# Optimization experiments

Hardware: AMD Instinct MI355X
Metric: run time of the kernel (lower is better)

## Reference

```python
import jax, jax.numpy as jnp
import numpy as np

# Config (matches init_kwargs defaults): V=25 joints, C=16 -> D=400, heads=2,
# ffn=64*25=1600, window L=9, stride=1, postnorm, gelu, dropout ignored (eval).
N, C, T, V = 16, 16, 300, 25
D = C * V          # 400
H = 2              # nhead
FF = 64 * V        # 1600
L = 9              # trans_length
MAX_LEN = 301


def _layernorm(x, g, b, eps=1e-5):
    mu = jnp.mean(x, axis=-1, keepdims=True)
    var = jnp.mean(jnp.square(x - mu), axis=-1, keepdims=True)
    return (x - mu) * jax.lax.rsqrt(var + eps) * g + b


def setup_inputs() -> dict:
    key = jax.random.key(0)
    ks = jax.random.split(key, 12)
    s = 0.02
    return {
        "x": jax.random.normal(ks[0], (N, C, T, V), jnp.float32),
        "pe": jax.random.normal(ks[1], (1, MAX_LEN, D), jnp.float32) * s,
        "w_in": jax.random.normal(ks[2], (3 * D, D), jnp.float32) * s,
        "b_in": jnp.zeros((3 * D,), jnp.float32),
        "w_out": jax.random.normal(ks[3], (D, D), jnp.float32) * s,
        "b_out": jnp.zeros((D,), jnp.float32),
        "w1": jax.random.normal(ks[4], (FF, D), jnp.float32) * s,
        "b1": jnp.zeros((FF,), jnp.float32),
        "w2": jax.random.normal(ks[5], (D, FF), jnp.float32) * s,
        "b2": jnp.zeros((D,), jnp.float32),
        "ln1_g": jnp.ones((D,), jnp.float32),
        "ln1_b": jnp.zeros((D,), jnp.float32),
        "ln2_g": jnp.ones((D,), jnp.float32),
        "ln2_b": jnp.zeros((D,), jnp.float32),
    }


def _encoder_layer(h, w_in, b_in, w_out, b_out, w1, b1, w2, b2,
                   ln1_g, ln1_b, ln2_g, ln2_b):
    # h: [B, L, D]; post-norm TransformerEncoderLayer (torch default)
    B, Lw, Dm = h.shape
    dh = Dm // H
    qkv = h @ w_in.T + b_in                             # [B,L,3D]
    q, k, v = jnp.split(qkv, 3, axis=-1)
    def heads(t):
        return t.reshape(B, Lw, H, dh).transpose(0, 2, 1, 3)  # [B,H,L,dh]
    q, k, v = heads(q), heads(k), heads(v)
    scores = jnp.einsum('bhqd,bhkd->bhqk', q, k) / np.float32(np.sqrt(dh))
    att = jax.nn.softmax(scores, axis=-1)
    o = jnp.einsum('bhqk,bhkd->bhqd', att, v)
    o = o.transpose(0, 2, 1, 3).reshape(B, Lw, Dm) @ w_out.T + b_out
    h = _layernorm(h + o, ln1_g, ln1_b)
    ff = jax.nn.gelu(h @ w1.T + b1, approximate=False) @ w2.T + b2
    return _layernorm(h + ff, ln2_g, ln2_b)


def reference(x, pe, w_in, b_in, w_out, b_out, w1, b1, w2, b2,
              ln1_g, ln1_b, ln2_g, ln2_b):
    n, c, t, v = x.shape
    d = c * v
    # [N,C,T,V] -> [N,T,V,C] -> [N,T,D]  (flatten order is (V,C), as in torch view)
    xs = x.transpose(0, 2, 3, 1).reshape(n, t, d)
    xs = xs + pe[:, :t, :]
    W = t - L                                            # number of windows (stride=1)
    win = jnp.arange(W)
    idx = win[:, None] + jnp.arange(L)[None, :]          # [W,L] gather indices
    xw = xs[:, idx, :].reshape(n * W, L, d)              # batched windows
    out = _encoder_layer(xw, w_in, b_in, w_out, b_out, w1, b1, w2, b2,
                         ln1_g, ln1_b, ln2_g, ln2_b)
    out = out.reshape(n, W * L, d)
    # window i writes into rows i//2 : i//2 + L and results are summed
    pos = ((win // 2)[:, None] + jnp.arange(L)[None, :]).reshape(-1)  # [W*L]
    xt = jnp.zeros((n, t, d), xs.dtype).at[:, pos, :].add(out)
    # [N,T,D] -> [N,T,V,C] -> [N,C,T,V]
    return xt.reshape(n, t, v, c).transpose(0, 3, 1, 2)
```

## Files before the change

kernel.cpp:

```cpp
#include <hip/hip_runtime.h>
#include <cstdint>
#include <cstddef>

#define N_    16
#define C_    16
#define T_    300
#define V_    25
#define D_    400
#define H_    2
#define DH_   200
#define FF_   1600
#define L_    9
#define W_    291
#define NW_   (N_*W_)
#define NT_   (N_*T_)

#define KP_   416
#define SD_   400
#define SQKV_ 1200
#define SFF_  1600

#define WIN_OFF   0u
#define WOUT_OFF  1064960u
#define W1_OFF    1490944u
#define W2_OFF    2981888u
#define XS_OFF    4620288u
#define QKV_OFF   8511488u
#define Z_OFF     20185088u
#define HEAD_END  53708288u

#define WAIT_VM3   0xF73
#define WAIT_VM0   0xF70

using u16 = unsigned short;
using u32 = unsigned int;
using frag  = __attribute__((ext_vector_type(8))) short;
using f32x4 = __attribute__((ext_vector_type(4))) float;

__device__ __forceinline__ float bf2f(u16 u){
  return __uint_as_float(((u32)u) << 16);
}
__device__ __forceinline__ u16 f2bf(float f){
  return (u16)((__float_as_uint(f) + 0x8000u) >> 16);
}
__device__ __forceinline__ u16 f2h(float f){
  _Float16 h = (_Float16)f;
  return *(u16*)&h;
}
__device__ __forceinline__ float h2f(u16 u){
  _Float16 h = *(_Float16*)&u;
  return (float)h;
}
__device__ __forceinline__ float gelu_f(float v){
  float s = __expf(-1.702f * v);
  return v * __builtin_amdgcn_rcpf(1.f + s);
}
__device__ __forceinline__ void unpack8(uint4 v, float* o){
  o[0] = bf2f((u16)(v.x & 0xffffu)); o[1] = bf2f((u16)(v.x >> 16));
  o[2] = bf2f((u16)(v.y & 0xffffu)); o[3] = bf2f((u16)(v.y >> 16));
  o[4] = bf2f((u16)(v.z & 0xffffu)); o[5] = bf2f((u16)(v.z >> 16));
  o[6] = bf2f((u16)(v.w & 0xffffu)); o[7] = bf2f((u16)(v.w >> 16));
}

__device__ __forceinline__ void convw_body(const float* src, u16* dst,
                                           int dN, int dK, int sN, int sK, int idx){
  if (idx >= dN * dK) return;
  int n = idx / dK, k = idx % dK;
  dst[idx] = (n < sN && k < sK) ? f2bf(src[(size_t)n * sK + k]) : (u16)0;
}

#define PREP_GRID 13824
__global__ __launch_bounds__(256) void prep_kernel(const float* __restrict__ x,
                                                   const float* __restrict__ pe,
                                                   const float* __restrict__ w_in,
                                                   const float* __restrict__ w_out,
                                                   const float* __restrict__ w1,
                                                   const float* __restrict__ w2,
                                                   u16* __restrict__ xs,
                                                   u16* __restrict__ w_in_b,
                                                   u16* __restrict__ w_out_b,
                                                   u16* __restrict__ w1_b,
                                                   u16* __restrict__ w2_b){
  __shared__ float xv[400];
  int b = blockIdx.x;
  int tid = threadIdx.x;
  if (b < 4800){
    int t = b % T_, n = b / T_;
    for (int i = tid; i < 400; i += 256){
      int c = i / 25, v = i - c*25;
      xv[i] = x[(((size_t)(n*C_ + c))*T_ + t)*V_ + v];
    }
    __syncthreads();
    for (int d = tid; d < 400; d += 256){
      float val = xv[(d & 15)*25 + (d >> 4)] + pe[t*D_ + d];
      xs[(size_t)b * D_ + d] = f2bf(val);
    }
  } else if (b < 6880){
    convw_body(w_in,  w_in_b,  1280, KP_, 1200, D_,  (b - 4800) * 256 + tid);
  } else if (b < 7712){
    convw_body(w_out, w_out_b,  512, KP_,  400, D_,  (b - 6880) * 256 + tid);
  } else if (b < 10624){
    convw_body(w1,    w1_b,   1792, KP_, 1600, D_,  (b - 7712) * 256 + tid);
  } else {
    convw_body(w2,    w2_b,    512, SFF_, 400, FF_, (b - 10624) * 256 + tid);
  }
}

template<int ACT>
__global__ __launch_bounds__(512) void gemm_mfma(const u16* __restrict__ A, int lda,
                                                 const u16* __restrict__ B, int ldb,
                                                 const float* __restrict__ bias,
                                                 u16* __restrict__ C, int ldc,
                                                 int Nn, int KPd,
                                                 int gx, int gy){
  __shared__ u16 smem[36864];
  int id = blockIdx.x;
  int c  = id & 7, t = id >> 3;
  int bx = t % gx;
  int by = (t / gx) * 8 + c;
  if (by >= gy) return;
  const int m0 = by * 128, n0 = bx * 256;

  const int tid  = threadIdx.x;
  const int lane = tid & 63;
  const int wv   = tid >> 6;
  const int quad = lane >> 4, l16 = lane & 15;
  const int wm   = wv & 1,   wn  = wv >> 1;

  const int srow = tid >> 2;
  const int sseg = (tid & 3) ^ ((tid >> 3) & 3);
  const u16* Ag = A + (size_t)(m0 + srow) * lda + sseg*8;
  const u16* Bg = B + (size_t)(n0 + srow) * ldb + sseg*8;

  f32x4 acc[4][4] = {};
  const int sa = quad ^ ((l16 >> 1) & 3);

  auto stage = [&](int buf, int kt){
    __builtin_amdgcn_global_load_lds(
        (const __attribute__((address_space(1))) void*)(Ag + kt),
        (__attribute__((address_space(3))) void*)(&smem[buf*4096 + wv*512]), 16, 0, 0);
    __builtin_amdgcn_global_load_lds(
        (const __attribute__((address_space(1))) void*)(Bg + kt),
        (__attribute__((address_space(3))) void*)(&smem[12288 + buf*8192 + wv*512]), 16, 0, 0);
    __builtin_amdgcn_global_load_lds(
        (const __attribute__((address_space(1))) void*)(Bg + kt + (size_t)128*ldb),
        (__attribute__((address_space(3))) void*)(&smem[12288 + buf*8192 + 4096 + wv*512]), 16, 0, 0);
  };

  const int nit = KPd >> 5;
  stage(0, 0);
  stage(1, 32);
  int nb = 2;
  for (int it = 0; it < nit; ++it){
    if (it < nit - 1) __builtin_amdgcn_s_waitcnt(WAIT_VM3);
    else              __builtin_amdgcn_s_waitcnt(WAIT_VM0);
    __builtin_amdgcn_s_barrier();
    if (it + 2 < nit){
      stage(nb, (it + 2) << 5);
      nb = (nb == 2) ? 0 : nb + 1;
    }
    const int buf = it % 3;
    const u16* Ar = &smem[buf*4096];
    const u16* Br = &smem[12288 + buf*8192];
    frag af[4], bfr[4];
    #pragma unroll
    for (int i = 0; i < 4; ++i)
      af[i]  = *(const frag*)(&Ar[(wm*64 + i*16 + l16)*32 + sa*8]);
    #pragma unroll
    for (int j = 0; j < 4; ++j)
      bfr[j] = *(const frag*)(&Br[(wn*64 + j*16 + l16)*32 + sa*8]);
    #pragma unroll
    for (int i = 0; i < 4; ++i)
      #pragma unroll
      for (int j = 0; j < 4; ++j)
        acc[i][j] = __builtin_amdgcn_mfma_f32_16x16x32_bf16(af[i], bfr[j], acc[i][j], 0, 0, 0);
  }

  __builtin_amdgcn_s_barrier();

  u16* ep = &smem[wv * 4608];
  #pragma unroll
  for (int j = 0; j < 4; ++j){
    int n = n0 + wn*64 + j*16 + l16;
    float bj = (n < Nn) ? bias[n] : 0.f;
    #pragma unroll
    for (int i = 0; i < 4; ++i){
      #pragma unroll
      for (int r = 0; r < 4; ++r){
        float v = acc[i][j][r] + bj;
        if (ACT) v = gelu_f(v);
        ep[(i*16 + quad*4 + r)*72 + j*16 + l16] = f2bf(v);
      }
    }
  }
  #pragma unroll
  for (int p = 0; p < 8; ++p){
    int row = p*8 + (lane >> 3);
    int seg = lane & 7;
    int nc  = n0 + wn*64 + seg*8;
    if (nc < Nn){
      uint4 v = *(const uint4*)(&ep[row*72 + seg*8]);
      *(uint4*)(C + (size_t)(m0 + wm*64 + row)*ldc + nc) = v;
    }
  }
}

__global__ __launch_bounds__(512) void gemm_ff2(const u16* __restrict__ A, int lda,
                                                const u16* __restrict__ B, int ldb,
                                                const float* __restrict__ bias,
                                                u16* __restrict__ C0, u16* __restrict__ C1,
                                                int ldc, int Nn, int KH,
                                                int gx, int gy, int Mr){
  __shared__ u16 smem[36864];
  int id = blockIdx.x;
  int c  = id & 7, t = id >> 3;
  int bxp = t % (2*gx);
  int by  = (t / (2*gx)) * 8 + c;
  if (by >= gy) return;
  const int half = (bxp >= gx) ? 1 : 0;
  const int bx   = bxp - half*gx;
  const int m0 = by * 128, n0 = bx * 256;
  const int koff = half * KH;
  u16* C = half ? C1 : C0;

  const int tid  = threadIdx.x;
  const int lane = tid & 63;
  const int wv   = tid >> 6;
  const int quad = lane >> 4, l16 = lane & 15;
  const int wm   = wv & 1,   wn  = wv >> 1;

  const int srow = tid >> 2;
  const int sseg = (tid & 3) ^ ((tid >> 3) & 3);
  const u16* Ag = A + (size_t)(m0 + srow) * lda + koff + sseg*8;
  const u16* Bg = B + (size_t)(n0 + srow) * ldb + koff + sseg*8;

  f32x4 acc[4][4] = {};
  const int sa = quad ^ ((l16 >> 1) & 3);

  auto stage = [&](int buf, int kt){
    __builtin_amdgcn_global_load_lds(
        (const __attribute__((address_space(1))) void*)(Ag + kt),
        (__attribute__((address_space(3))) void*)(&smem[buf*4096 + wv*512]), 16, 0, 0);
    __builtin_amdgcn_global_load_lds(
        (const __attribute__((address_space(1))) void*)(Bg + kt),
        (__attribute__((address_space(3))) void*)(&smem[12288 + buf*8192 + wv*512]), 16, 0, 0);
    __builtin_amdgcn_global_load_lds(
        (const __attribute__((address_space(1))) void*)(Bg + kt + (size_t)128*ldb),
        (__attribute__((address_space(3))) void*)(&smem[12288 + buf*8192 + 4096 + wv*512]), 16, 0, 0);
  };

  const int nit = KH >> 5;
  stage(0, 0);
  stage(1, 32);
  int nb = 2;
  for (int it = 0; it < nit; ++it){
    if (it < nit - 1) __builtin_amdgcn_s_waitcnt(WAIT_VM3);
    else              __builtin_amdgcn_s_waitcnt(WAIT_VM0);
    __builtin_amdgcn_s_barrier();
    if (it + 2 < nit){
      stage(nb, (it + 2) << 5);
      nb = (nb == 2) ? 0 : nb + 1;
    }
    const int buf = it % 3;
    const u16* Ar = &smem[buf*4096];
    const u16* Br = &smem[12288 + buf*8192];
    frag af[4], bfr[4];
    #pragma unroll
    for (int i = 0; i < 4; ++i)
      af[i]  = *(const frag*)(&Ar[(wm*64 + i*16 + l16)*32 + sa*8]);
    #pragma unroll
    for (int j = 0; j < 4; ++j)
      bfr[j] = *(const frag*)(&Br[(wn*64 + j*16 + l16)*32 + sa*8]);
    #pragma unroll
    for (int i = 0; i < 4; ++i)
      #pragma unroll
      for (int j = 0; j < 4; ++j)
        acc[i][j] = __builtin_amdgcn_mfma_f32_16x16x32_bf16(af[i], bfr[j], acc[i][j], 0, 0, 0);
  }

  __builtin_amdgcn_s_barrier();

  u16* ep = &smem[wv * 4608];
  #pragma unroll
  for (int j = 0; j < 4; ++j){
    int n = n0 + wn*64 + j*16 + l16;
    float bj = (!half && n < Nn) ? bias[n] : 0.f;
    #pragma unroll
    for (int i = 0; i < 4; ++i){
      #pragma unroll
      for (int r = 0; r < 4; ++r){
        float v = acc[i][j][r] + bj;
        ep[(i*16 + quad*4 + r)*72 + j*16 + l16] = f2bf(v);
      }
    }
  }
  #pragma unroll
  for (int p = 0; p < 8; ++p){
    int row = p*8 + (lane >> 3);
    int seg = lane & 7;
    int nc  = n0 + wn*64 + seg*8;
    int mr  = m0 + wm*64 + row;
    if (nc < Nn && mr < Mr){
      uint4 v = *(const uint4*)(&ep[row*72 + seg*8]);
      *(uint4*)(C + (size_t)mr*ldc + nc) = v;
    }
  }
}

#define WB_     8
#define ATT_NB  37
#define ATT_GRID (N_ * ATT_NB)
__global__ __launch_bounds__(256) void attn_kernel(const u16* __restrict__ qkv,
                                                   u16* __restrict__ o,
                                                   int g0, int gend){
  __shared__ u16 kv[20480];
  __shared__ float att[WB_ * 2 * 81];
  const int b  = blockIdx.x;
  const int n  = b / ATT_NB;
  const int w0 = (b - n * ATT_NB) * WB_;
  const int gbase = n * W_ + w0;
  if (gbase >= gend || gbase + WB_ <= g0) return;

  const int tid  = threadIdx.x;
  const int lane = tid & 63;
  const int wv   = tid >> 6;

  const char* gsrc = (const char*)(qkv + (size_t)(n * T_ + w0) * SQKV_);
  #pragma unroll
  for (int j = 0; j < 10; ++j){
    __builtin_amdgcn_global_load_lds(
        (const __attribute__((address_space(1))) void*)(gsrc + j*4096 + wv*1024 + lane*16),
        (__attribute__((address_space(3))) void*)((char*)kv + j*4096 + wv*1024),
        16, 0, 0);
  }
  __builtin_amdgcn_s_waitcnt(WAIT_VM0);
  __syncthreads();

  for (int i = tid; i < WB_ * 162; i += 256){
    int w  = i / 162;
    int r  = i - w * 162;
    int h  = r / 81;
    int p  = r - h * 81;
    int qi = p / 9, ki = p - qi * 9;
    const u16* qp = kv + (w + qi) * 1200 + h * DH_;
    const u16* kp = kv + (w + ki) * 1200 + D_ + h * DH_;
    float s = 0.f;
    #pragma unroll 5
    for (int cch = 0; cch < 25; ++cch){
      float qa[8], kb[8];
      unpack8(*(const uint4*)(qp + cch*8), qa);
      unpack8(*(const uint4*)(kp + cch*8), kb);
      #pragma unroll
      for (int e = 0; e < 8; ++e) s += qa[e] * kb[e];
    }
    att[i] = s * 0.07071067811865475f;
  }
  __syncthreads();

  if (tid < WB_ * 18){
    float* row = att + tid * 9;
    float mx = row[0];
    #pragma unroll
    for (int j = 1; j < 9; ++j) mx = fmaxf(mx, row[j]);
    float e[9]; float sum = 0.f;
    #pragma unroll
    for (int j = 0; j < 9; ++j){ e[j] = __expf(row[j] - mx); sum += e[j]; }
    float inv = 1.f / sum;
    #pragma unroll
    for (int j = 0; j < 9; ++j) row[j] = e[j] * inv;
  }
  __syncthreads();

  for (int i = tid; i < WB_ * 900; i += 256){
    int w  = i / 900;
    int r  = i - w * 900;
    int l  = r / 100;
    int c4 = r - l * 100;
    int h  = (c4 >= 50) ? 1 : 0;
    const float* ap = att + (w*2 + h)*81 + l*9;
    float o4[4] = {0.f, 0.f, 0.f, 0.f};
    #pragma unroll
    for (int ki = 0; ki < 9; ++ki){
      float a = ap[ki];
      uint2 vv = *(const uint2*)(kv + (w + ki)*1200 + 2*D_ + c4*4);
      o4[0] += a * bf2f((u16)(vv.x & 0xffffu));
      o4[1] += a * bf2f((u16)(vv.x >> 16));
      o4[2] += a * bf2f((u16)(vv.y & 0xffffu));
      o4[3] += a * bf2f((u16)(vv.y >> 16));
    }
    int g = gbase + w;
    if (w0 + w < W_ && g >= g0 && g < gend){
      u32 lo = (u32)f2bf(o4[0]) | ((u32)f2bf(o4[1]) << 16);
      u32 hi = (u32)f2bf(o4[2]) | ((u32)f2bf(o4[3]) << 16);
      *(uint2*)(o + ((size_t)(g - g0) * L_ + l) * SD_ + c4*4) = make_uint2(lo, hi);
    }
  }
}

__global__ __launch_bounds__(256) void ln1_kernel(const u16* __restrict__ y,
                                                  const float* __restrict__ gam,
                                                  const float* __restrict__ bet,
                                                  u16* __restrict__ out,
                                                  const u16* __restrict__ xs,
                                                  int g0){
  const int wv = threadIdx.x >> 6, lane = threadIdx.x & 63;
  const int r = blockIdx.x * 4 + wv;
  const int g = g0 + r / L_, l = r % L_;
  const int n = g / W_, w = g % W_;
  const u16* arow = xs + ((size_t)(n*T_ + w + l)) * SD_;
  const u16* brow = y + (size_t)r * SD_;

  const bool act = lane < 50;
  float v[8];
  float s = 0.f, s2 = 0.f;
  if (act){
    float a8[8], b8[8];
    unpack8(*(const uint4*)(arow + lane*8), a8);
    unpack8(*(const uint4*)(brow + lane*8), b8);
    #pragma unroll
    for (int i = 0; i < 8; ++i){ v[i] = a8[i] + b8[i]; s += v[i]; s2 += v[i]*v[i]; }
  } else {
    #pragma unroll
    for (int i = 0; i < 8; ++i) v[i] = 0.f;
  }
  #pragma unroll
  for (int off = 32; off; off >>= 1){
    s  += __shfl_xor(s,  off);
    s2 += __shfl_xor(s2, off);
  }
  float mean = s * (1.f / D_);
  float rstd = rsqrtf(s2 * (1.f / D_) - mean*mean + 1e-5f);
  if (act){
    float4 ga = *(const float4*)(gam + lane*8);
    float4 gb = *(const float4*)(gam + lane*8 + 4);
    float4 ba = *(const float4*)(bet + lane*8);
    float4 bb = *(const float4*)(bet + lane*8 + 4);
    float gg[8] = {ga.x,ga.y,ga.z,ga.w, gb.x,gb.y,gb.z,gb.w};
    float bb8[8]= {ba.x,ba.y,ba.z,ba.w, bb.x,bb.y,bb.z,bb.w};
    u32 o4[4];
    #pragma unroll
    for (int i = 0; i < 4; ++i){
      u16 lo = f2bf((v[2*i]   - mean) * rstd * gg[2*i]   + bb8[2*i]);
      u16 hi = f2bf((v[2*i+1] - mean) * rstd * gg[2*i+1] + bb8[2*i+1]);
      o4[i] = (u32)lo | ((u32)hi << 16);
    }
    *(uint4*)(out + (size_t)r * SD_ + lane*8) = make_uint4(o4[0],o4[1],o4[2],o4[3]);
  }
}

__global__ __launch_bounds__(256) void ln2_gather(const u16* __restrict__ h,
                                                  const u16* __restrict__ y,
                                                  const u16* __restrict__ y2,
                                                  const float* __restrict__ gam,
                                                  const float* __restrict__ bet,
                                                  float* __restrict__ dout){
  __shared__ float buf[4][400];
  const int b = blockIdx.x;
  const int t = b % T_;
  const int n = b / T_;
  const int wv = threadIdx.x >> 6, lane = threadIdx.x & 63;
  const bool act = lane < 50;

  float gg[8], bb8[8];
  if (act){
    float4 ga = *(const float4*)(gam + lane*8);
    float4 gb = *(const float4*)(gam + lane*8 + 4);
    float4 ba = *(const float4*)(bet + lane*8);
    float4 bb = *(const float4*)(bet + lane*8 + 4);
    gg[0]=ga.x; gg[1]=ga.y; gg[2]=ga.z; gg[3]=ga.w;
    gg[4]=gb.x; gg[5]=gb.y; gg[6]=gb.z; gg[7]=gb.w;
    bb8[0]=ba.x; bb8[1]=ba.y; bb8[2]=ba.z; bb8[3]=ba.w;
    bb8[4]=bb.x; bb8[5]=bb.y; bb8[6]=bb.z; bb8[7]=bb.w;
  }
  float racc[8] = {0.f,0.f,0.f,0.f,0.f,0.f,0.f,0.f};

  for (int idx = wv; idx < 18; idx += 4){
    int l  = idx >> 1;
    int dt = t - l;
    if (dt < 0 || dt > 145) continue;
    int w = dt * 2 + (idx & 1);
    if (w >= W_) continue;
    size_t r = ((size_t)(n * W_ + w)) * L_ + l;
    const u16* arow = h + r * SD_;
    const u16* brow = y + r * SD_;
    const u16* crow = y2 + r * SD_;
    float v[8];
    float s = 0.f, s2 = 0.f;
    if (act){
      float a8[8], b8[8], c8[8];
      unpack8(*(const uint4*)(arow + lane*8), a8);
      unpack8(*(const uint4*)(brow + lane*8), b8);
      unpack8(*(const uint4*)(crow + lane*8), c8);
      #pragma unroll
      for (int i = 0; i < 8; ++i){ v[i] = a8[i] + b8[i] + c8[i]; s += v[i]; s2 += v[i]*v[i]; }
    } else {
      #pragma unroll
      for (int i = 0; i < 8; ++i) v[i] = 0.f;
    }
    #pragma unroll
    for (int off = 32; off; off >>= 1){
      s  += __shfl_xor(s,  off);
      s2 += __shfl_xor(s2, off);
    }
    float mean = s * (1.f / D_);
    float rstd = rsqrtf(s2 * (1.f / D_) - mean*mean + 1e-5f);
    if (act){
      #pragma unroll
      for (int i = 0; i < 8; ++i)
        racc[i] += (v[i] - mean) * rstd * gg[i] + bb8[i];
    }
  }
  if (act){
    #pragma unroll
    for (int i = 0; i < 8; ++i) buf[wv][lane*8 + i] = racc[i];
  }
  __syncthreads();
  for (int d = threadIdx.x; d < D_; d += 256){
    float s = buf[0][d] + buf[1][d] + buf[2][d] + buf[3][d];
    dout[(((size_t)(n*C_ + (d & 15)))*T_ + t)*V_ + (d >> 4)] = s;
  }
}

__global__ __launch_bounds__(256) void ln2z_kernel(const u16* __restrict__ h,
                                                   const u16* __restrict__ y,
                                                   const float* __restrict__ gam,
                                                   const float* __restrict__ bet,
                                                   u16* __restrict__ z,
                                                   int g0){
  const int wv = threadIdx.x >> 6, lane = threadIdx.x & 63;
  const int r = blockIdx.x * 4 + wv;
  const u16* arow = h + (size_t)r * SD_;
  const u16* brow = y + (size_t)r * SD_;

  const bool act = lane < 50;
  float v[8];
  float s = 0.f, s2 = 0.f;
  if (act){
    float a8[8], b8[8];
    unpack8(*(const uint4*)(arow + lane*8), a8);
    unpack8(*(const uint4*)(brow + lane*8), b8);
    #pragma unroll
    for (int i = 0; i < 8; ++i){ v[i] = a8[i] + b8[i]; s += v[i]; s2 += v[i]*v[i]; }
  } else {
    #pragma unroll
    for (int i = 0; i < 8; ++i) v[i] = 0.f;
  }
  #pragma unroll
  for (int off = 32; off; off >>= 1){
    s  += __shfl_xor(s,  off);
    s2 += __shfl_xor(s2, off);
  }
  float mean = s * (1.f / D_);
  float rstd = rsqrtf(s2 * (1.f / D_) - mean*mean + 1e-5f);
  if (act){
    float4 ga = *(const float4*)(gam + lane*8);
    float4 gb = *(const float4*)(gam + lane*8 + 4);
    float4 ba = *(const float4*)(bet + lane*8);
    float4 bb = *(const float4*)(bet + lane*8 + 4);
    float gg[8] = {ga.x,ga.y,ga.z,ga.w, gb.x,gb.y,gb.z,gb.w};
    float bb8[8]= {ba.x,ba.y,ba.z,ba.w, bb.x,bb.y,bb.z,bb.w};
    u32 o4[4];
    #pragma unroll
    for (int i = 0; i < 4; ++i){
      u16 lo = f2h((v[2*i]   - mean) * rstd * gg[2*i]   + bb8[2*i]);
      u16 hi = f2h((v[2*i+1] - mean) * rstd * gg[2*i+1] + bb8[2*i+1]);
      o4[i] = (u32)lo | ((u32)hi << 16);
    }
    *(uint4*)(z + ((size_t)(g0 * L_) + r) * SD_ + lane*8) = make_uint4(o4[0],o4[1],o4[2],o4[3]);
  }
}

__global__ __launch_bounds__(256) void gather_final(const u16* __restrict__ z,
                                                    float* __restrict__ dout){
  int idx = blockIdx.x * 256 + threadIdx.x;
  if (idx >= NT_ * D_) return;
  int d  = idx % D_;
  int nt = idx / D_;
  int t  = nt % T_;
  int n  = nt / T_;
  float s = 0.f;
  #pragma unroll
  for (int l = 0; l < L_; ++l){
    int dt = t - l;
    if (dt >= 0 && dt <= 145){
      int w = dt * 2;
      const u16* zp = z + ((size_t)((n*W_ + w)*L_ + l)) * SD_ + d;
      s += h2f(zp[0]);
      if (w + 1 < W_) s += h2f(zp[(size_t)L_ * SD_]);
    }
  }
  dout[(((size_t)(n*C_ + (d & 15)))*T_ + t)*V_ + (d >> 4)] = s;
}

extern "C" void kernel_launch(void* const* d_in, const int* in_sizes, int n_in,
                              void* d_out, int out_size, void* d_ws, size_t ws_size,
                              hipStream_t stream){
  (void)in_sizes; (void)n_in; (void)out_size;
  const float* x     = (const float*)d_in[0];
  const float* pe    = (const float*)d_in[1];
  const float* w_in  = (const float*)d_in[2];
  const float* b_in  = (const float*)d_in[3];
  const float* w_out = (const float*)d_in[4];
  const float* b_out = (const float*)d_in[5];
  const float* w1    = (const float*)d_in[6];
  const float* b1    = (const float*)d_in[7];
  const float* w2    = (const float*)d_in[8];
  const float* b2    = (const float*)d_in[9];
  const float* ln1g  = (const float*)d_in[10];
  const float* ln1b  = (const float*)d_in[11];
  const float* ln2g  = (const float*)d_in[12];
  const float* ln2b  = (const float*)d_in[13];

  int nch = 3;
  {
    size_t need1 = (size_t)HEAD_END + (size_t)41984 * 4800;
    size_t need2 = (size_t)HEAD_END + (size_t)20992 * 4800;
    if (ws_size >= need1 + (1u<<20)) nch = 1;
    else if (ws_size >= need2 + (1u<<20)) nch = 2;
  }
  const int CW  = NW_ / nch;
  const int RC  = CW * L_;
  const int RCP = ((RC + 127) / 128) * 128;

  char* ws = (char*)d_ws;
  u16*   w_in_b  = (u16*)(ws + WIN_OFF);
  u16*   w_out_b = (u16*)(ws + WOUT_OFF);
  u16*   w1_b    = (u16*)(ws + W1_OFF);
  u16*   w2_b    = (u16*)(ws + W2_OFF);
  u16*   xs      = (u16*)(ws + XS_OFF);
  u16*   qkv     = (u16*)(ws + QKV_OFF);
  u16*   z       = (u16*)(ws + Z_OFF);
  u16*   y2      = (u16*)(ws + Z_OFF);
  u16*   y_c     = (u16*)(ws + HEAD_END);
  u16*   h_c     = y_c + (size_t)RCP * SD_;
  u16*   ffc     = h_c + (size_t)RCP * SD_;
  u16*   o_c     = ffc;

  prep_kernel<<<PREP_GRID, 256, 0, stream>>>(x, pe, w_in, w_out, w1, w2,
                                             xs, w_in_b, w_out_b, w1_b, w2_b);

  {
    int gx = 5, gy = (NT_ + 127)/128, gy8 = (gy + 7) & ~7;
    gemm_mfma<0><<<gx*gy8, 512, 0, stream>>>(
        xs, SD_, w_in_b, KP_, b_in, qkv, SQKV_, 1200, KP_, gx, gy);
  }

  const int gyc = RCP/128, gyc8 = (gyc + 7) & ~7;

  for (int g0 = 0; g0 < NW_; g0 += CW){
    attn_kernel<<<ATT_GRID, 256, 0, stream>>>(qkv, o_c, g0, g0 + CW);

    gemm_mfma<0><<<2*gyc8, 512, 0, stream>>>(
        o_c, SD_, w_out_b, KP_, b_out, y_c, SD_, D_, KP_, 2, gyc);

    ln1_kernel<<<RC/4, 256, 0, stream>>>(y_c, ln1g, ln1b, h_c, xs, g0);

    gemm_mfma<1><<<7*gyc8, 512, 0, stream>>>(
        h_c, SD_, w1_b, KP_, b1, ffc, SFF_, FF_, KP_, 7, gyc);

    if (nch == 1){
      gemm_ff2<<<4*gyc8, 512, 0, stream>>>(
          ffc, SFF_, w2_b, SFF_, b2, y_c, y2, SD_, D_, 800, 2, gyc, RC);
    } else {
      gemm_mfma<0><<<2*gyc8, 512, 0, stream>>>(
          ffc, SFF_, w2_b, SFF_, b2, y_c, SD_, D_, SFF_, 2, gyc);
      ln2z_kernel<<<RC/4, 256, 0, stream>>>(h_c, y_c, ln2g, ln2b, z, g0);
    }
  }

  if (nch == 1)
    ln2_gather<<<NT_, 256, 0, stream>>>(h_c, y_c, y2, ln2g, ln2b, (float*)d_out);
  else
    gather_final<<<(NT_*D_ + 255)/256, 256, 0, stream>>>(z, (float*)d_out);
}
```

Measured before the change: 364.5 us.

## Fuse out-projection GEMM with residual LayerNorm; drop split-K FF2 path

Replaces the split-K FF2 kernel with a new kernel that computes the attention output projection over full 128x512 tiles (all 400 columns per block), stages the result in LDS and applies residual add with xs plus LayerNorm1 in the epilogue. This removes the y_c round trip and the separate ln1 launch. The FF2 GEMM reverts to the plain non-split kernel, so ln2_gather now reads two inputs instead of three. The fused kernel uses more LDS and fewer, larger blocks, which lowers occupancy, and dropping split-K may cost FF2 parallelism.

```diff
diff --git a/kernel.cpp b/kernel.cpp
--- a/kernel.cpp
+++ b/kernel.cpp
@@ -29,6 +29,7 @@
 #define Z_OFF     20185088u
 #define HEAD_END  53708288u
 
+#define WAIT_VM10  0xF7A
 #define WAIT_VM3   0xF73
 #define WAIT_VM0   0xF70
 
@@ -205,23 +206,20 @@
   }
 }
 
-__global__ __launch_bounds__(512) void gemm_ff2(const u16* __restrict__ A, int lda,
-                                                const u16* __restrict__ B, int ldb,
-                                                const float* __restrict__ bias,
-                                                u16* __restrict__ C0, u16* __restrict__ C1,
-                                                int ldc, int Nn, int KH,
-                                                int gx, int gy, int Mr){
-  __shared__ u16 smem[36864];
+__global__ __launch_bounds__(512) void gemm_wout_ln1(const u16* __restrict__ A, int lda,
+                                                     const u16* __restrict__ B, int ldb,
+                                                     const float* __restrict__ bias,
+                                                     const u16* __restrict__ xs,
+                                                     const float* __restrict__ gam,
+                                                     const float* __restrict__ bet,
+                                                     u16* __restrict__ hout,
+                                                     int Mr, int KPd, int gy){
+  __shared__ u16 smem[61440];
   int id = blockIdx.x;
   int c  = id & 7, t = id >> 3;
-  int bxp = t % (2*gx);
-  int by  = (t / (2*gx)) * 8 + c;
+  int by = t * 8 + c;
   if (by >= gy) return;
-  const int half = (bxp >= gx) ? 1 : 0;
-  const int bx   = bxp - half*gx;
-  const int m0 = by * 128, n0 = bx * 256;
-  const int koff = half * KH;
-  u16* C = half ? C1 : C0;
+  const int m0 = by * 128;
 
   const int tid  = threadIdx.x;
   const int lane = tid & 63;
@@ -231,30 +229,30 @@
 
   const int srow = tid >> 2;
   const int sseg = (tid & 3) ^ ((tid >> 3) & 3);
-  const u16* Ag = A + (size_t)(m0 + srow) * lda + koff + sseg*8;
-  const u16* Bg = B + (size_t)(n0 + srow) * ldb + koff + sseg*8;
-
-  f32x4 acc[4][4] = {};
+  const u16* Ag = A + (size_t)(m0 + srow) * lda + sseg*8;
+  const u16* Bg = B + (size_t)srow * ldb + sseg*8;
+
+  f32x4 acc[4][8] = {};
   const int sa = quad ^ ((l16 >> 1) & 3);
 
   auto stage = [&](int buf, int kt){
     __builtin_amdgcn_global_load_lds(
         (const __attribute__((address_space(1))) void*)(Ag + kt),
         (__attribute__((address_space(3))) void*)(&smem[buf*4096 + wv*512]), 16, 0, 0);
-    __builtin_amdgcn_global_load_lds(
-        (const __attribute__((address_space(1))) void*)(Bg + kt),
-        (__attribute__((address_space(3))) void*)(&smem[12288 + buf*8192 + wv*512]), 16, 0, 0);
-    __builtin_amdgcn_global_load_lds(
-        (const __attribute__((address_space(1))) void*)(Bg + kt + (size_t)128*ldb),
-        (__attribute__((address_space(3))) void*)(&smem[12288 + buf*8192 + 4096 + wv*512]), 16, 0, 0);
+    #pragma unroll
+    for (int ch = 0; ch < 4; ++ch){
+      __builtin_amdgcn_global_load_lds(
+          (const __attribute__((address_space(1))) void*)(Bg + kt + (size_t)(128*ch)*ldb),
+          (__attribute__((address_space(3))) void*)(&smem[12288 + buf*16384 + ch*4096 + wv*512]), 16, 0, 0);
+    }
   };
 
-  const int nit = KH >> 5;
+  const int nit = KPd >> 5;
   stage(0, 0);
   stage(1, 32);
   int nb = 2;
   for (int it = 0; it < nit; ++it){
-    if (it < nit - 1) __builtin_amdgcn_s_waitcnt(WAIT_VM3);
+    if (it < nit - 1) __builtin_amdgcn_s_waitcnt(WAIT_VM10);
     else              __builtin_amdgcn_s_waitcnt(WAIT_VM0);
     __builtin_amdgcn_s_barrier();
     if (it + 2 < nit){
@@ -263,46 +261,91 @@
     }
     const int buf = it % 3;
     const u16* Ar = &smem[buf*4096];
-    const u16* Br = &smem[12288 + buf*8192];
-    frag af[4], bfr[4];
+    const u16* Br = &smem[12288 + buf*16384];
+    frag af[4];
     #pragma unroll
     for (int i = 0; i < 4; ++i)
-      af[i]  = *(const frag*)(&Ar[(wm*64 + i*16 + l16)*32 + sa*8]);
-    #pragma unroll
-    for (int j = 0; j < 4; ++j)
-      bfr[j] = *(const frag*)(&Br[(wn*64 + j*16 + l16)*32 + sa*8]);
-    #pragma unroll
-    for (int i = 0; i < 4; ++i)
+      af[i] = *(const frag*)(&Ar[(wm*64 + i*16 + l16)*32 + sa*8]);
+    #pragma unroll
+    for (int jh = 0; jh < 2; ++jh){
+      frag bfr[4];
       #pragma unroll
       for (int j = 0; j < 4; ++j)
-        acc[i][j] = __builtin_amdgcn_mfma_f32_16x16x32_bf16(af[i], bfr[j], acc[i][j], 0, 0, 0);
+        bfr[j] = *(const frag*)(&Br[(wn*128 + (jh*4+j)*16 + l16)*32 + sa*8]);
+      #pragma unroll
+      for (int i = 0; i < 4; ++i)
+        #pragma unroll
+        for (int j = 0; j < 4; ++j)
+          acc[i][jh*4+j] = __builtin_amdgcn_mfma_f32_16x16x32_bf16(af[i], bfr[j], acc[i][jh*4+j], 0, 0, 0);
+    }
   }
 
   __builtin_amdgcn_s_barrier();
 
-  u16* ep = &smem[wv * 4608];
+  u16* ep = smem;
   #pragma unroll
-  for (int j = 0; j < 4; ++j){
-    int n = n0 + wn*64 + j*16 + l16;
-    float bj = (!half && n < Nn) ? bias[n] : 0.f;
-    #pragma unroll
-    for (int i = 0; i < 4; ++i){
-      #pragma unroll
-      for (int r = 0; r < 4; ++r){
-        float v = acc[i][j][r] + bj;
-        ep[(i*16 + quad*4 + r)*72 + j*16 + l16] = f2bf(v);
+  for (int j = 0; j < 8; ++j){
+    int nc = wn*128 + j*16 + l16;
+    if (nc < 400){
+      float bj = bias[nc];
+      #pragma unroll
+      for (int i = 0; i < 4; ++i){
+        #pragma unroll
+        for (int r = 0; r < 4; ++r){
+          ep[(wm*64 + i*16 + quad*4 + r)*408 + nc] = f2bf(acc[i][j][r] + bj);
+        }
       }
     }
   }
-  #pragma unroll
-  for (int p = 0; p < 8; ++p){
-    int row = p*8 + (lane >> 3);
-    int seg = lane & 7;
-    int nc  = n0 + wn*64 + seg*8;
-    int mr  = m0 + wm*64 + row;
-    if (nc < Nn && mr < Mr){
-      uint4 v = *(const uint4*)(&ep[row*72 + seg*8]);
-      *(uint4*)(C + (size_t)mr*ldc + nc) = v;
+  __syncthreads();
+
+  const bool act = lane < 50;
+  float gg[8], bb8[8];
+  if (act){
+    float4 ga = *(const float4*)(gam + lane*8);
+    float4 gb = *(const float4*)(gam + lane*8 + 4);
+    float4 ba = *(const float4*)(bet + lane*8);
+    float4 bb = *(const float4*)(bet + lane*8 + 4);
+    gg[0]=ga.x; gg[1]=ga.y; gg[2]=ga.z; gg[3]=ga.w;
+    gg[4]=gb.x; gg[5]=gb.y; gg[6]=gb.z; gg[7]=gb.w;
+    bb8[0]=ba.x; bb8[1]=ba.y; bb8[2]=ba.z; bb8[3]=ba.w;
+    bb8[4]=bb.x; bb8[5]=bb.y; bb8[6]=bb.z; bb8[7]=bb.w;
+  }
+  for (int rr = 0; rr < 16; ++rr){
+    int row = wv*16 + rr;
+    int rg  = m0 + row;
+    if (rg >= Mr) break;
+    int g = rg / L_, l = rg - g*L_;
+    int n = g / W_, w = g - n*W_;
+    const u16* arow = xs + ((size_t)(n*T_ + w + l)) * SD_;
+    float v[8];
+    float s = 0.f, s2 = 0.f;
+    if (act){
+      float a8[8], b8[8];
+      unpack8(*(const uint4*)(arow + lane*8), a8);
+      unpack8(*(const uint4*)(&ep[row*408 + lane*8]), b8);
+      #pragma unroll
+      for (int i = 0; i < 8; ++i){ v[i] = a8[i] + b8[i]; s += v[i]; s2 += v[i]*v[i]; }
+    } else {
+      #pragma unroll
+      for (int i = 0; i < 8; ++i) v[i] = 0.f;
+    }
+    #pragma unroll
+    for (int off = 32; off; off >>= 1){
+      s  += __shfl_xor(s,  off);
+      s2 += __shfl_xor(s2, off);
+    }
+    float mean = s * (1.f / D_);
+    float rstd = rsqrtf(s2 * (1.f / D_) - mean*mean + 1e-5f);
+    if (act){
+      u32 o4[4];
+      #pragma unroll
+      for (int i = 0; i < 4; ++i){
+        u16 lo = f2bf((v[2*i]   - mean) * rstd * gg[2*i]   + bb8[2*i]);
+        u16 hi = f2bf((v[2*i+1] - mean) * rstd * gg[2*i+1] + bb8[2*i+1]);
+        o4[i] = (u32)lo | ((u32)hi << 16);
+      }
+      *(uint4*)(hout + (size_t)rg * SD_ + lane*8) = make_uint4(o4[0],o4[1],o4[2],o4[3]);
     }
   }
 }
@@ -450,7 +493,6 @@
 
 __global__ __launch_bounds__(256) void ln2_gather(const u16* __restrict__ h,
                                                   const u16* __restrict__ y,
-                                                  const u16* __restrict__ y2,
                                                   const float* __restrict__ gam,
                                                   const float* __restrict__ bet,
                                                   float* __restrict__ dout){
@@ -483,16 +525,14 @@
     size_t r = ((size_t)(n * W_ + w)) * L_ + l;
     const u16* arow = h + r * SD_;
     const u16* brow = y + r * SD_;
-    const u16* crow = y2 + r * SD_;
     float v[8];
     float s = 0.f, s2 = 0.f;
     if (act){
-      float a8[8], b8[8], c8[8];
+      float a8[8], b8[8];
       unpack8(*(const uint4*)(arow + lane*8), a8);
       unpack8(*(const uint4*)(brow + lane*8), b8);
-      unpack8(*(const uint4*)(crow + lane*8), c8);
-      #pragma unroll
-      for (int i = 0; i < 8; ++i){ v[i] = a8[i] + b8[i] + c8[i]; s += v[i]; s2 += v[i]*v[i]; }
+      #pragma unroll
+      for (int i = 0; i < 8; ++i){ v[i] = a8[i] + b8[i]; s += v[i]; s2 += v[i]*v[i]; }
     } else {
       #pragma unroll
       for (int i = 0; i < 8; ++i) v[i] = 0.f;
@@ -630,7 +670,6 @@
   u16*   xs      = (u16*)(ws + XS_OFF);
   u16*   qkv     = (u16*)(ws + QKV_OFF);
   u16*   z       = (u16*)(ws + Z_OFF);
-  u16*   y2      = (u16*)(ws + Z_OFF);
   u16*   y_c     = (u16*)(ws + HEAD_END);
   u16*   h_c     = y_c + (size_t)RCP * SD_;
   u16*   ffc     = h_c + (size_t)RCP * SD_;
@@ -650,26 +689,27 @@
   for (int g0 = 0; g0 < NW_; g0 += CW){
     attn_kernel<<<ATT_GRID, 256, 0, stream>>>(qkv, o_c, g0, g0 + CW);
 
-    gemm_mfma<0><<<2*gyc8, 512, 0, stream>>>(
-        o_c, SD_, w_out_b, KP_, b_out, y_c, SD_, D_, KP_, 2, gyc);
-
-    ln1_kernel<<<RC/4, 256, 0, stream>>>(y_c, ln1g, ln1b, h_c, xs, g0);
+    if (nch == 1){
+      gemm_wout_ln1<<<gyc8, 512, 0, stream>>>(
+          o_c, SD_, w_out_b, KP_, b_out, xs, ln1g, ln1b, h_c, RC, KP_, gyc);
+    } else {
+      gemm_mfma<0><<<2*gyc8, 512, 0, stream>>>(
+          o_c, SD_, w_out_b, KP_, b_out, y_c, SD_, D_, KP_, 2, gyc);
+      ln1_kernel<<<RC/4, 256, 0, stream>>>(y_c, ln1g, ln1b, h_c, xs, g0);
+    }
 
     gemm_mfma<1><<<7*gyc8, 512, 0, stream>>>(
         h_c, SD_, w1_b, KP_, b1, ffc, SFF_, FF_, KP_, 7, gyc);
 
-    if (nch == 1){
-      gemm_ff2<<<4*gyc8, 512, 0, stream>>>(
-          ffc, SFF_, w2_b, SFF_, b2, y_c, y2, SD_, D_, 800, 2, gyc, RC);
-    } else {
-      gemm_mfma<0><<<2*gyc8, 512, 0, stream>>>(
-          ffc, SFF_, w2_b, SFF_, b2, y_c, SD_, D_, SFF_, 2, gyc);
+    gemm_mfma<0><<<2*gyc8, 512, 0, stream>>>(
+        ffc, SFF_, w2_b, SFF_, b2, y_c, SD_, D_, SFF_, 2, gyc);
+
+    if (nch > 1)
       ln2z_kernel<<<RC/4, 256, 0, stream>>>(h_c, y_c, ln2g, ln2b, z, g0);
-    }
   }
 
   if (nch == 1)
-    ln2_gather<<<NT_, 256, 0, stream>>>(h_c, y_c, y2, ln2g, ln2b, (float*)d_out);
+    ln2_gather<<<NT_, 256, 0, stream>>>(h_c, y_c, ln2g, ln2b, (float*)d_out);
   else
     gather_final<<<(NT_*D_ + 255)/256, 256, 0, stream>>>(z, (float*)d_out);
 }
```

New measurement: 374.9 us. 2.9% more time.
